# Optimization experiments

Hardware: AMD Instinct MI355X
Metric: run time of the kernel (lower is better)

Reference implementation:

```python
import jax, jax.numpy as jnp
import numpy as np

MAX_LEN = 128
VOCAB = 32000
SENTINEL = 2**30  # larger than any valid token id; pushes masked slots to the end after sort


def setup_inputs() -> dict:
    key = jax.random.key(0)
    k1, k2, k3, k4 = jax.random.split(key, 4)
    B, L = 262144, MAX_LEN
    input_ids = jax.random.randint(k1, (B, L), 0, VOCAB, dtype=jnp.int32)
    attention_mask = jax.random.randint(k2, (B, L), 0, 2, dtype=jnp.int32)
    # MLP params: Linear(3,32) -> ReLU -> Linear(32,32) -> ReLU
    W1 = jax.random.normal(k3, (3, 32), dtype=jnp.float32) * (1.0 / np.sqrt(3.0))
    b1 = jnp.zeros((32,), dtype=jnp.float32)
    W2 = jax.random.normal(k4, (32, 32), dtype=jnp.float32) * (1.0 / np.sqrt(32.0))
    b2 = jnp.zeros((32,), dtype=jnp.float32)
    return {"input_ids": input_ids, "attention_mask": attention_mask,
            "W1": W1, "b1": b1, "W2": W2, "b2": b2}


def _symbolic_feats(input_ids, attention_mask):
    # Batched replacement of the per-row torch.unique loop:
    # sort masked tokens per row, count boundaries between distinct values.
    mask = attention_mask.astype(bool)
    seq_len = jnp.sum(mask, axis=1)  # [B]
    ids_m = jnp.where(mask, input_ids, SENTINEL)  # masked-out slots -> sentinel
    s = jnp.sort(ids_m, axis=1)  # valid tokens first (ids < SENTINEL)
    valid = s < SENTINEL
    first = jnp.ones((s.shape[0], 1), dtype=bool)
    new_val = jnp.concatenate([first, s[:, 1:] != s[:, :-1]], axis=1)
    uniq = jnp.sum(valid & new_val, axis=1)  # [B] unique count among valid tokens
    seq_f = seq_len.astype(jnp.float32)
    uniq_f = uniq.astype(jnp.float32)
    uniq_ratio = jnp.where(seq_len > 0, uniq_f / jnp.maximum(seq_f, 1.0), 0.0)
    feats = jnp.stack([seq_f / MAX_LEN, uniq_f / MAX_LEN, uniq_ratio], axis=1)  # [B,3]
    return feats


def reference(input_ids, attention_mask, W1, b1, W2, b2):
    feats = _symbolic_feats(input_ids, attention_mask)  # [B,3]
    h = jax.nn.relu(feats @ W1 + b1)
    out = jax.nn.relu(h @ W2 + b2)
    return out
```

## Files before the change

### kernel.cpp

```cpp
#include <hip/hip_runtime.h>

#define ROW_LEN 128
#define NPAIR (129 * 129)

__global__ __launch_bounds__(256) void mlp_table_kernel(
    const float* __restrict__ W1, const float* __restrict__ b1,
    const float* __restrict__ W2, const float* __restrict__ b2,
    float* __restrict__ table)
{
    const int tid = blockIdx.x * 256 + threadIdx.x;
    if (tid >= NPAIR * 32) return;
    const int p = tid >> 5;
    const int j = tid & 31;
    const int seq  = p / 129;
    const int uniq = p % 129;
    const float f0 = (float)seq  * (1.0f / 128.0f);
    const float f1 = (float)uniq * (1.0f / 128.0f);
    const float f2 = (seq > 0) ? ((float)uniq / (float)seq) : 0.0f;

    float acc = b2[j];
    #pragma unroll
    for (int jj = 0; jj < 32; ++jj) {
        float h = b1[jj];
        h = fmaf(f0, W1[jj],      h);
        h = fmaf(f1, W1[32 + jj], h);
        h = fmaf(f2, W1[64 + jj], h);
        h = fmaxf(h, 0.0f);
        acc = fmaf(h, W2[jj * 32 + j], acc);
    }
    table[tid] = fmaxf(acc, 0.0f);
}

__global__ __launch_bounds__(256, 8) void rows_kernel(
    const int* __restrict__ ids, const int* __restrict__ amask,
    const float* __restrict__ table, float* __restrict__ out, int B)
{
    __shared__ unsigned bm[4][1024];

    const int wave = threadIdx.x >> 6;
    const int lane = threadIdx.x & 63;
    const long row = (long)blockIdx.x * 4 + wave;
    if (row >= B) return;

    const long v = row * 64 + lane;
    const int2 id2 = ((const int2*)ids)[v];
    const int2 mk2 = ((const int2*)amask)[v];

    uint4* z = (uint4*)bm[wave];
    #pragma unroll
    for (int i = 0; i < 4; ++i) z[lane + i * 64] = make_uint4(0u, 0u, 0u, 0u);
    unsigned* mybm = bm[wave];

    int n0 = 0, n1 = 0;
    if (mk2.x != 0) {
        const unsigned t = (unsigned)id2.x, m = 1u << (t & 31u);
        n0 = ((atomicOr(&mybm[t >> 5], m) & m) == 0u);
    }
    if (mk2.y != 0) {
        const unsigned t = (unsigned)id2.y, m = 1u << (t & 31u);
        n1 = ((atomicOr(&mybm[t >> 5], m) & m) == 0u);
    }

    const unsigned long long s0 = __ballot(mk2.x != 0);
    const unsigned long long s1 = __ballot(mk2.y != 0);
    const unsigned long long u0 = __ballot(n0 != 0);
    const unsigned long long u1 = __ballot(n1 != 0);

    const int seq  = __popcll(s0) + __popcll(s1);
    const int uniq = __popcll(u0) + __popcll(u1);

    const int p = seq * 129 + uniq;
    if (lane < 32) out[row * 32 + lane] = table[p * 32 + lane];
}

extern "C" void kernel_launch(void* const* d_in, const int* in_sizes, int n_in,
                              void* d_out, int out_size, void* d_ws, size_t ws_size,
                              hipStream_t stream) {
    const int*   ids   = (const int*)d_in[0];
    const int*   amask = (const int*)d_in[1];
    const float* W1    = (const float*)d_in[2];
    const float* b1    = (const float*)d_in[3];
    const float* W2    = (const float*)d_in[4];
    const float* b2    = (const float*)d_in[5];
    float* out   = (float*)d_out;
    float* table = (float*)d_ws;

    const int B = in_sizes[0] / ROW_LEN;

    const int tblThreads = NPAIR * 32;
    mlp_table_kernel<<<(tblThreads + 255) / 256, 256, 0, stream>>>(W1, b1, W2, b2, table);

    rows_kernel<<<(B + 3) / 4, 256, 0, stream>>>(ids, amask, table, out, B);
}
```

Before: 280.6 us.

## Replace zeroed LDS bitmap with hash table and ballot-based collision resolution

Each wave now scatters its lane index into a 1024-entry LDS hash table keyed by the token's low bits. A lane whose index survives counts as a unique winner. Lanes that lose are resolved in a ballot/readlane loop that checks whether any winner holds the same token. This removes the 4KB per-wave bitmap clearing and the LDS atomics, at the cost of a data-dependent loop whose length grows with hash collisions. The occupancy hint on launch bounds is also dropped.

```diff
diff --git a/kernel.cpp b/kernel.cpp
--- a/kernel.cpp
+++ b/kernel.cpp
@@ -2,6 +2,7 @@
 
 #define ROW_LEN 128
 #define NPAIR (129 * 129)
+#define TBL 1024
 
 __global__ __launch_bounds__(256) void mlp_table_kernel(
     const float* __restrict__ W1, const float* __restrict__ b1,
@@ -31,11 +32,11 @@
     table[tid] = fmaxf(acc, 0.0f);
 }
 
-__global__ __launch_bounds__(256, 8) void rows_kernel(
+__global__ __launch_bounds__(256) void rows_kernel(
     const int* __restrict__ ids, const int* __restrict__ amask,
     const float* __restrict__ table, float* __restrict__ out, int B)
 {
-    __shared__ unsigned bm[4][1024];
+    __shared__ unsigned tb[4][TBL];
 
     const int wave = threadIdx.x >> 6;
     const int lane = threadIdx.x & 63;
@@ -46,28 +47,44 @@
     const int2 id2 = ((const int2*)ids)[v];
     const int2 mk2 = ((const int2*)amask)[v];
 
-    uint4* z = (uint4*)bm[wave];
-    #pragma unroll
-    for (int i = 0; i < 4; ++i) z[lane + i * 64] = make_uint4(0u, 0u, 0u, 0u);
-    unsigned* mybm = bm[wave];
+    volatile unsigned* t = tb[wave];
 
-    int n0 = 0, n1 = 0;
-    if (mk2.x != 0) {
-        const unsigned t = (unsigned)id2.x, m = 1u << (t & 31u);
-        n0 = ((atomicOr(&mybm[t >> 5], m) & m) == 0u);
+    const bool mx = (mk2.x != 0);
+    const bool my = (mk2.y != 0);
+    const unsigned hx = ((unsigned)id2.x) & (TBL - 1);
+    const unsigned hy = ((unsigned)id2.y) & (TBL - 1);
+
+    if (mx) t[hx] = (unsigned)lane;
+    if (my) t[hy] = (unsigned)(64 + lane);
+
+    const unsigned r0 = t[hx];
+    const unsigned r1 = t[hy];
+
+    const bool win0 = mx && (r0 == (unsigned)lane);
+    const bool win1 = my && (r1 == (unsigned)(64 + lane));
+
+    const int seq = __popcll(__ballot(mx)) + __popcll(__ballot(my));
+    int uniq = __popcll(__ballot(win0)) + __popcll(__ballot(win1));
+
+    unsigned long long p0 = __ballot(mx && !win0);
+    unsigned long long p1 = __ballot(my && !win1);
+    while (p0 | p1) {
+        int T;
+        if (p0) {
+            const int l = __ffsll((long long)p0) - 1;
+            T = __builtin_amdgcn_readlane(id2.x, l);
+        } else {
+            const int l = __ffsll((long long)p1) - 1;
+            T = __builtin_amdgcn_readlane(id2.y, l);
+        }
+        const unsigned long long ex = __ballot(mx && (id2.x == T));
+        const unsigned long long ey = __ballot(my && (id2.y == T));
+        const unsigned long long w  = __ballot((win0 && (id2.x == T)) ||
+                                               (win1 && (id2.y == T)));
+        uniq += (w == 0ull);
+        p0 &= ~ex;
+        p1 &= ~ey;
     }
-    if (mk2.y != 0) {
-        const unsigned t = (unsigned)id2.y, m = 1u << (t & 31u);
-        n1 = ((atomicOr(&mybm[t >> 5], m) & m) == 0u);
-    }
-
-    const unsigned long long s0 = __ballot(mk2.x != 0);
-    const unsigned long long s1 = __ballot(mk2.y != 0);
-    const unsigned long long u0 = __ballot(n0 != 0);
-    const unsigned long long u1 = __ballot(n1 != 0);
-
-    const int seq  = __popcll(s0) + __popcll(s1);
-    const int uniq = __popcll(u0) + __popcll(u1);
 
     const int p = seq * 129 + uniq;
     if (lane < 32) out[row * 32 + lane] = table[p * 32 + lane];
```

New measurement: 287.9 us. +2.6%, slower.

## Persistent waves with prefetch and epoch-tagged hash table for unique counting

Applied to the files above, without the earlier changes.

Turns the row kernel into a grid-stride persistent kernel with 2048 blocks, where each wave loops over rows and prefetches the next row's ids and mask while working on the current one. The per-wave 32K-bit bitmap, which had to be zeroed for every row, is replaced by a 1024-entry table of epoch-tagged slots that is cleared only once per wave. Hash collisions are settled by a wave-wide loop using readlane and ballot. This removes the per-row clearing and launch overhead, but adds collision-handling work whose cost depends on how many tokens collide in a row.

```diff
diff --git a/kernel.cpp b/kernel.cpp
--- a/kernel.cpp
+++ b/kernel.cpp
@@ -2,6 +2,7 @@
 
 #define ROW_LEN 128
 #define NPAIR (129 * 129)
+#define TBL 1024
 
 __global__ __launch_bounds__(256) void mlp_table_kernel(
     const float* __restrict__ W1, const float* __restrict__ b1,
@@ -35,42 +36,73 @@
     const int* __restrict__ ids, const int* __restrict__ amask,
     const float* __restrict__ table, float* __restrict__ out, int B)
 {
-    __shared__ unsigned bm[4][1024];
+    __shared__ unsigned tb[4][TBL];
 
     const int wave = threadIdx.x >> 6;
     const int lane = threadIdx.x & 63;
-    const long row = (long)blockIdx.x * 4 + wave;
-    if (row >= B) return;
+    unsigned* t = tb[wave];
 
-    const long v = row * 64 + lane;
-    const int2 id2 = ((const int2*)ids)[v];
-    const int2 mk2 = ((const int2*)amask)[v];
-
-    uint4* z = (uint4*)bm[wave];
+    uint4* z = (uint4*)t;
     #pragma unroll
     for (int i = 0; i < 4; ++i) z[lane + i * 64] = make_uint4(0u, 0u, 0u, 0u);
-    unsigned* mybm = bm[wave];
 
-    int n0 = 0, n1 = 0;
-    if (mk2.x != 0) {
-        const unsigned t = (unsigned)id2.x, m = 1u << (t & 31u);
-        n0 = ((atomicOr(&mybm[t >> 5], m) & m) == 0u);
-    }
-    if (mk2.y != 0) {
-        const unsigned t = (unsigned)id2.y, m = 1u << (t & 31u);
-        n1 = ((atomicOr(&mybm[t >> 5], m) & m) == 0u);
+    const long gwave   = (long)blockIdx.x * 4 + wave;
+    const long wstride = (long)gridDim.x * 4;
+
+    long row = gwave;
+    int2 id2 = make_int2(0, 0), mk2 = make_int2(0, 0);
+    if (row < B) {
+        id2 = ((const int2*)ids)[row * 64 + lane];
+        mk2 = ((const int2*)amask)[row * 64 + lane];
     }
 
-    const unsigned long long s0 = __ballot(mk2.x != 0);
-    const unsigned long long s1 = __ballot(mk2.y != 0);
-    const unsigned long long u0 = __ballot(n0 != 0);
-    const unsigned long long u1 = __ballot(n1 != 0);
+    unsigned e = 1;
+    for (; row < B; row += wstride, ++e) {
+        const long nrow = row + wstride;
+        int2 id2n = make_int2(0, 0), mk2n = make_int2(0, 0);
+        if (nrow < B) {
+            id2n = ((const int2*)ids)[nrow * 64 + lane];
+            mk2n = ((const int2*)amask)[nrow * 64 + lane];
+        }
 
-    const int seq  = __popcll(s0) + __popcll(s1);
-    const int uniq = __popcll(u0) + __popcll(u1);
+        const bool mx = (mk2.x != 0);
+        const bool my = (mk2.y != 0);
+        const unsigned tx = (unsigned)id2.x;
+        const unsigned ty = (unsigned)id2.y;
+        const unsigned tagx = (e << 15) | tx;
+        const unsigned tagy = (e << 15) | ty;
 
-    const int p = seq * 129 + uniq;
-    if (lane < 32) out[row * 32 + lane] = table[p * 32 + lane];
+        unsigned rx = 0, ry = 0;
+        if (mx) rx = atomicExch(&t[tx & (TBL - 1)], tagx);
+        if (my) ry = atomicExch(&t[ty & (TBL - 1)], tagy);
+
+        const bool headx = mx && ((rx >> 15) != e);
+        const bool heady = my && ((ry >> 15) != e);
+        const bool dupx  = mx && !headx && ((rx & 0x7FFFu) == tx);
+        const bool dupy  = my && !heady && ((ry & 0x7FFFu) == ty);
+
+        const int seq = __popcll(__ballot(mx)) + __popcll(__ballot(my));
+        int uniq = __popcll(__ballot(headx)) + __popcll(__ballot(heady));
+
+        unsigned long long p0 = __ballot(mx && !headx && !dupx);
+        unsigned long long p1 = __ballot(my && !heady && !dupy);
+        while (p0 | p1) {
+            int T;
+            if (p0) T = __builtin_amdgcn_readlane(id2.x, __ffsll((long long)p0) - 1);
+            else    T = __builtin_amdgcn_readlane(id2.y, __ffsll((long long)p1) - 1);
+            const unsigned long long w =
+                __ballot((headx && id2.x == T) || (heady && id2.y == T));
+            uniq += (w == 0ull);
+            p0 &= ~__ballot(id2.x == T);
+            p1 &= ~__ballot(id2.y == T);
+        }
+
+        const int p = seq * 129 + uniq;
+        if (lane < 32) out[row * 32 + lane] = table[p * 32 + lane];
+
+        id2 = id2n;
+        mk2 = mk2n;
+    }
 }
 
 extern "C" void kernel_launch(void* const* d_in, const int* in_sizes, int n_in,
@@ -90,5 +122,5 @@
     const int tblThreads = NPAIR * 32;
     mlp_table_kernel<<<(tblThreads + 255) / 256, 256, 0, stream>>>(W1, b1, W2, b2, table);
 
-    rows_kernel<<<(B + 3) / 4, 256, 0, stream>>>(ids, amask, table, out, B);
+    rows_kernel<<<2048, 256, 0, stream>>>(ids, amask, table, out, B);
 }
```

New measurement: 297.8 us. +6.1%, slower.
